# Kernel tuning notes

Measured on AMD Instinct MI355X. Metric: run time of the kernel, lower is better.

The kernel has to match this reference:

```python
import jax, jax.numpy as jnp
import numpy as np

DIM, HEADS, K = 128, 4, 7
HD = DIM // HEADS


def _nbr_idx(n, k):
    # NATTEN boundary-clamped neighborhood (dilation=1): window start clamped to [0, n-k]
    i = np.arange(n)
    start = np.clip(i - k // 2, 0, n - k)
    idx = start[:, None] + np.arange(k)[None, :]          # (n, k) absolute neighbor index
    rel = idx - i[:, None] + (k - 1)                      # (n, k) index into 2k-1 rpb axis
    return jnp.asarray(idx), jnp.asarray(rel)


def _ln(x, w, b, eps=1e-5):
    mu = jnp.mean(x, -1, keepdims=True)
    var = jnp.var(x, -1, keepdims=True)
    return (x - mu) * jax.lax.rsqrt(var + eps) * w + b


def setup_inputs() -> dict:
    key = jax.random.key(0)
    ks = jax.random.split(key, 16)
    B, H, W, C = 1, 128, 128, DIM
    f = jax.random.normal
    inp = {
        'x': f(ks[0], (B, H, W, C), jnp.float32),
        'y': f(ks[1], (B, H, W, C), jnp.float32),
        'qv_w': f(ks[2], (2 * C, C), jnp.float32) * 0.02,
        'qv_b': jnp.zeros((2 * C,), jnp.float32),
        'k_w': f(ks[3], (C, C), jnp.float32) * 0.02,
        'k_b': jnp.zeros((C,), jnp.float32),
        'rpb': f(ks[4], (HEADS, 2 * K - 1, 2 * K - 1), jnp.float32) * 0.02,
        'proj_w': f(ks[5], (C, C), jnp.float32) * 0.02,
        'proj_b': jnp.zeros((C,), jnp.float32),
        'n1_w': jnp.ones((C,), jnp.float32),
        'n1_b': jnp.zeros((C,), jnp.float32),
        'n2_w': jnp.ones((C,), jnp.float32),
        'n2_b': jnp.zeros((C,), jnp.float32),
        'fc1_w': f(ks[6], (4 * C, C), jnp.float32) * 0.02,
        'fc1_b': jnp.zeros((4 * C,), jnp.float32),
        'fc2_w': f(ks[7], (C, 4 * C), jnp.float32) * 0.02,
        'fc2_b': jnp.zeros((C,), jnp.float32),
    }
    return inp


def _block(x, y, qv_w, qv_b, k_w, k_b, rpb, proj_w, proj_b,
           n1_w, n1_b, n2_w, n2_b, fc1_w, fc1_b, fc2_w, fc2_b):
    B, H, W, C = x.shape
    scale = HD ** -0.5
    # ---- CrossNat2D attention on norm1(x) vs y ----
    xn = _ln(x, n1_w, n1_b)
    qv = xn @ qv_w.T + qv_b                               # (B,H,W,2C)
    q = qv[..., :C].reshape(B, H, W, HEADS, HD) * scale
    v = qv[..., C:].reshape(B, H, W, HEADS, HD)
    k = (y @ k_w.T + k_b).reshape(B, H, W, HEADS, HD)

    idx_h, rel_h = _nbr_idx(H, K)
    idx_w, rel_w = _nbr_idx(W, K)
    # gather neighborhoods: (B, H, K, W, K, HEADS, HD)
    k_nbr = k[:, idx_h][:, :, :, idx_w]
    v_nbr = v[:, idx_h][:, :, :, idx_w]

    # attention logits over KxK neighborhood
    attn = jnp.einsum('bijhd,biajchd->bijhac', q, k_nbr)  # (B,H,W,heads,K,K)
    bias = rpb[:, rel_h][..., rel_w]                      # (heads,H,K,W,K)
    attn = attn + jnp.transpose(bias, (1, 3, 0, 2, 4))    # broadcast over B
    attn = jax.nn.softmax(attn.reshape(B, H, W, HEADS, K * K), axis=-1)
    attn = attn.reshape(B, H, W, HEADS, K, K)

    out = jnp.einsum('bijhac,biajchd->bijhd', attn, v_nbr).reshape(B, H, W, C)
    out = out @ proj_w.T + proj_b

    x = x + out
    # ---- MLP ----
    h = _ln(x, n2_w, n2_b) @ fc1_w.T + fc1_b
    h = jax.nn.gelu(h, approximate=False) @ fc2_w.T + fc2_b
    return x + h


def reference(x, y, qv_w, qv_b, k_w, k_b, rpb, proj_w, proj_b,
              n1_w, n1_b, n2_w, n2_b, fc1_w, fc1_b, fc2_w, fc2_b):
    return _block(x, y, qv_w, qv_b, k_w, k_b, rpb, proj_w, proj_b,
                  n1_w, n1_b, n2_w, n2_b, fc1_w, fc1_b, fc2_w, fc2_b)
```

## Files before the change

kernel.cpp:

```cpp
#include <hip/hip_runtime.h>
#include <hip/hip_bf16.h>


#define N_PIX 16384
#define C 128
#define HEADS 4
#define HD 32
#define HW 128

typedef __hip_bfloat16 bf16;
typedef __attribute__((ext_vector_type(8))) short bf16x8;
typedef __attribute__((ext_vector_type(4))) float f32x4;

__device__ __forceinline__ short f2bs(float f) {
    bf16 h = __float2bfloat16(f);
    return (short)__bfloat16_as_ushort(h);
}
__device__ __forceinline__ float bs2f(short s) {
    __hip_bfloat16_raw r; r.x = (unsigned short)s;
    return __bfloat162float(__hip_bfloat16(r));
}
__device__ __forceinline__ float gelu_f(float v) {
    const float z = 1.5957691216f * (v + 0.044715f * v * v * v);
    return v / (1.f + __expf(-z));
}
__device__ __forceinline__ unsigned int pack2(float a, float b) {
    return (unsigned int)(unsigned short)f2bs(a) |
           ((unsigned int)(unsigned short)f2bs(b) << 16);
}

__global__ __launch_bounds__(256) void k_wconv(
    const float* __restrict__ qv_w, const float* __restrict__ k_w,
    const float* __restrict__ proj_w, const float* __restrict__ fc1_w,
    const float* __restrict__ fc2_w,
    short* __restrict__ wqv, short* __restrict__ wk, short* __restrict__ wproj,
    short* __restrict__ wfc1, short* __restrict__ wfc2) {
    const int i = blockIdx.x * 256 + threadIdx.x;
    if (i < 32768) wqv[i] = f2bs(qv_w[i]);
    if (i < 16384) { wk[i] = f2bs(k_w[i]); wproj[i] = f2bs(proj_w[i]); }
    if (i < 65536) { wfc1[i] = f2bs(fc1_w[i]); wfc2[i] = f2bs(fc2_w[i]); }
}

__global__ __launch_bounds__(256, 4) void k_qkv(
    const float* __restrict__ x, const float* __restrict__ y,
    const short* __restrict__ wqv, const float* __restrict__ qv_b,
    const short* __restrict__ wk, const float* __restrict__ k_b,
    const float* __restrict__ n1_w, const float* __restrict__ n1_b,
    bf16* __restrict__ qb, bf16* __restrict__ vb, bf16* __restrict__ kb) {
    __shared__ float xr[16][132];
    __shared__ short xn[16][136];
    __shared__ short yl[16][136];
    __shared__ float muA[16], riA[16];
    const int t = threadIdx.x;
    const int pix0 = (blockIdx.x & 7) * 2048 + (blockIdx.x >> 3) * 16;
    for (int e = t; e < 512; e += 256) {
        const int r = e >> 5, c4 = (e & 31) * 4;
        const float4 xv = *(const float4*)(x + (size_t)(pix0 + r) * C + c4);
        *(float4*)&xr[r][c4] = xv;
        const float4 yv = *(const float4*)(y + (size_t)(pix0 + r) * C + c4);
        uint2 yp; yp.x = pack2(yv.x, yv.y); yp.y = pack2(yv.z, yv.w);
        *(uint2*)&yl[r][c4] = yp;
    }
    __syncthreads();
    if (t < 128) {
        const int r = t >> 3, s = t & 7;
        float sm = 0.f, sq = 0.f;
        for (int i = 0; i < 16; i++) { float v = xr[r][s * 16 + i]; sm += v; sq += v * v; }
        for (int m = 1; m < 8; m <<= 1) { sm += __shfl_xor(sm, m, 64); sq += __shfl_xor(sq, m, 64); }
        if (s == 0) {
            const float mu = sm * (1.f / 128.f);
            const float var = sq * (1.f / 128.f) - mu * mu;
            muA[r] = mu; riA[r] = rsqrtf(var + 1e-5f);
        }
    }
    __syncthreads();
    for (int e = t; e < 2048; e += 256) {
        const int r = e >> 7, c = e & 127;
        xn[r][c] = f2bs((xr[r][c] - muA[r]) * riA[r] * n1_w[c] + n1_b[c]);
    }
    __syncthreads();
    const int wave = t >> 6, lane = t & 63, quad = lane >> 4, l15 = lane & 15;
    const float scale = 0.1767766952966369f;
    {
        bf16x8 aA[4];
#pragma unroll
        for (int kt = 0; kt < 4; kt++)
            aA[kt] = *(const bf16x8*)&xn[l15][kt * 32 + quad * 8];
#pragma unroll
        for (int s = 0; s < 4; s++) {
            const int n = (wave * 4 + s) * 16 + l15;
            f32x4 acc = {0.f, 0.f, 0.f, 0.f};
#pragma unroll
            for (int kt = 0; kt < 4; kt++) {
                bf16x8 b = *(const bf16x8*)&wqv[n * C + kt * 32 + quad * 8];
                acc = __builtin_amdgcn_mfma_f32_16x16x32_bf16(aA[kt], b, acc, 0, 0, 0);
            }
            const float bias = qv_b[n];
#pragma unroll
            for (int r = 0; r < 4; r++) {
                const int m = quad * 4 + r;
                const float v = acc[r] + bias;
                if (n < C) qb[(size_t)(pix0 + m) * C + n] = __float2bfloat16(v * scale);
                else       vb[(size_t)(pix0 + m) * C + (n - C)] = __float2bfloat16(v);
            }
        }
    }
    {
        bf16x8 aY[4];
#pragma unroll
        for (int kt = 0; kt < 4; kt++)
            aY[kt] = *(const bf16x8*)&yl[l15][kt * 32 + quad * 8];
        const int n0 = (wave * 2) * 16 + l15, n1 = (wave * 2 + 1) * 16 + l15;
        f32x4 a0 = {0.f, 0.f, 0.f, 0.f}, a1 = {0.f, 0.f, 0.f, 0.f};
#pragma unroll
        for (int kt = 0; kt < 4; kt++) {
            bf16x8 b0 = *(const bf16x8*)&wk[n0 * C + kt * 32 + quad * 8];
            bf16x8 b1 = *(const bf16x8*)&wk[n1 * C + kt * 32 + quad * 8];
            a0 = __builtin_amdgcn_mfma_f32_16x16x32_bf16(aY[kt], b0, a0, 0, 0, 0);
            a1 = __builtin_amdgcn_mfma_f32_16x16x32_bf16(aY[kt], b1, a1, 0, 0, 0);
        }
        const float b0s = k_b[n0], b1s = k_b[n1];
#pragma unroll
        for (int r = 0; r < 4; r++) {
            const int m = quad * 4 + r;
            kb[(size_t)(pix0 + m) * C + n0] = __float2bfloat16(a0[r] + b0s);
            kb[(size_t)(pix0 + m) * C + n1] = __float2bfloat16(a1[r] + b1s);
        }
    }
}

__global__ __launch_bounds__(256, 3) void k_attn(
    const bf16* __restrict__ qb, const bf16* __restrict__ kb,
    const bf16* __restrict__ vb, const float* __restrict__ rpb,
    const float* __restrict__ x,
    const short* __restrict__ wproj, const float* __restrict__ proj_b,
    float* __restrict__ out) {
    __shared__ short U[112 * 132];
    __shared__ short Pb[64 * 120];
    __shared__ short aoL[16 * 136];
    const int t = threadIdx.x;
    const int wave = t >> 6, lane = t & 63, quad = lane >> 4, l15 = lane & 15;
    const int h = wave;
    const int tile = (blockIdx.x & 7) * 128 + (blockIdx.x >> 3);
    const int i0 = (tile >> 5) * 4, j0 = (tile & 31) * 4;
    const int rs = min(max(i0 - 3, 0), 118);
    const int cs = min(max(j0 - 3, 0), 118);
    const int pA = (i0 + (l15 >> 2)) * HW + j0 + (l15 & 3);
    const bf16x8 aQ = *(const bf16x8*)(qb + (size_t)pA * C + h * HD + quad * 8);
    const int nR0 = h * 16 + l15, nR1 = (h + 4) * 16 + l15;
    float xres0[4], xres1[4];
#pragma unroll
    for (int r = 0; r < 4; r++) {
        const int m = quad * 4 + r;
        const int p = (i0 + (m >> 2)) * HW + j0 + (m & 3);
        xres0[r] = x[(size_t)p * C + nR0];
        xres1[r] = x[(size_t)p * C + nR1];
    }
    uint4 vst[7];
#pragma unroll
    for (int it = 0; it < 7; ++it) {
        const int u = t + it * 256;
        const int r = u >> 4, seg = u & 15;
        const int sr = min(r, 99);
        const size_t g = (size_t)((rs + sr / 10) * HW + cs + sr % 10) * C + seg * 8;
        *(uint4*)&U[r * 132 + seg * 8] = *(const uint4*)(kb + g);
        vst[it] = *(const uint4*)(vb + g);
    }
    __syncthreads();
    f32x4 S[7];
#pragma unroll
    for (int nt = 0; nt < 7; nt++) {
        const bf16x8 bK = *(const bf16x8*)&U[(nt * 16 + l15) * 132 + h * HD + quad * 8];
        f32x4 z = {0.f, 0.f, 0.f, 0.f};
        S[nt] = __builtin_amdgcn_mfma_f32_16x16x32_bf16(aQ, bK, z, 0, 0, 0);
    }
    __syncthreads();
#pragma unroll
    for (int it = 0; it < 7; ++it) {
        const int u = t + it * 256;
        const int r = u >> 4, seg = u & 15;
        *(uint4*)&U[r * 132 + seg * 8] = vst[it];
    }
    const float* rpbh = rpb + h * 169;
    int aiA[7], ajA[7];
#pragma unroll
    for (int nt = 0; nt < 7; nt++) {
        const int nb = nt * 16 + l15;
        aiA[nt] = rs + nb / 10;
        ajA[nt] = cs + nb % 10;
    }
    float smx[4];
#pragma unroll
    for (int r = 0; r < 4; r++) {
        const int m = quad * 4 + r;
        const int i = i0 + (m >> 2), j = j0 + (m & 3);
        const int shi = min(max(i - 3, 0), 121);
        const int swj = min(max(j - 3, 0), 121);
        float best = -1e30f;
#pragma unroll
        for (int nt = 0; nt < 7; nt++) {
            const int nb = nt * 16 + l15;
            const int ai = aiA[nt], aj = ajA[nt];
            const bool valid = (nb < 100) & (ai >= shi) & (ai <= shi + 6) & (aj >= swj) & (aj <= swj + 6);
            const int ri = min(max(ai - i + 6, 0), 12);
            const int rj = min(max(aj - j + 6, 0), 12);
            const float v = valid ? (S[nt][r] + rpbh[ri * 13 + rj]) : -1e30f;
            S[nt][r] = v;
            best = fmaxf(best, v);
        }
        for (int msk = 1; msk < 16; msk <<= 1) best = fmaxf(best, __shfl_xor(best, msk, 64));
        float s = 0.f;
#pragma unroll
        for (int nt = 0; nt < 7; nt++) {
            const float e = __expf(S[nt][r] - best);
            S[nt][r] = e;
            s += e;
        }
        for (int msk = 1; msk < 16; msk <<= 1) s += __shfl_xor(s, msk, 64);
        smx[r] = 1.f / s;
    }
#pragma unroll
    for (int r = 0; r < 4; r++) {
        short* prow = &Pb[(h * 16 + quad * 4 + r) * 120];
#pragma unroll
        for (int nt = 0; nt < 7; nt++) prow[nt * 16 + l15] = f2bs(S[nt][r] * smx[r]);
    }
    __syncthreads();
    f32x4 O0 = {0.f, 0.f, 0.f, 0.f}, O1 = {0.f, 0.f, 0.f, 0.f};
#pragma unroll
    for (int kt = 0; kt < 3; kt++) {
        const bf16x8 aP = *(const bf16x8*)&Pb[(h * 16 + l15) * 120 + kt * 32 + quad * 8];
#pragma unroll
        for (int nt2 = 0; nt2 < 2; nt2++) {
            const int ch = h * HD + nt2 * 16 + l15;
            const int base = (kt * 32 + quad * 8) * 132 + ch;
            bf16x8 bV;
#pragma unroll
            for (int jj = 0; jj < 8; jj++) bV[jj] = U[base + jj * 132];
            if (nt2 == 0) O0 = __builtin_amdgcn_mfma_f32_16x16x32_bf16(aP, bV, O0, 0, 0, 0);
            else          O1 = __builtin_amdgcn_mfma_f32_16x16x32_bf16(aP, bV, O1, 0, 0, 0);
        }
    }
    {
        bf16x8 aP = {0, 0, 0, 0, 0, 0, 0, 0};
        if (quad < 2) aP = *(const bf16x8*)&Pb[(h * 16 + l15) * 120 + 96 + quad * 8];
#pragma unroll
        for (int nt2 = 0; nt2 < 2; nt2++) {
            const int ch = h * HD + nt2 * 16 + l15;
            bf16x8 bV = {0, 0, 0, 0, 0, 0, 0, 0};
            if (quad < 2) {
                const int base = (96 + quad * 8) * 132 + ch;
#pragma unroll
                for (int jj = 0; jj < 8; jj++) bV[jj] = U[base + jj * 132];
            }
            if (nt2 == 0) O0 = __builtin_amdgcn_mfma_f32_16x16x32_bf16(aP, bV, O0, 0, 0, 0);
            else          O1 = __builtin_amdgcn_mfma_f32_16x16x32_bf16(aP, bV, O1, 0, 0, 0);
        }
    }
#pragma unroll
    for (int r = 0; r < 4; r++) {
        const int m = quad * 4 + r;
        aoL[m * 136 + h * HD + l15] = f2bs(O0[r]);
        aoL[m * 136 + h * HD + 16 + l15] = f2bs(O1[r]);
    }
    __syncthreads();
    bf16x8 aO[4];
#pragma unroll
    for (int kt = 0; kt < 4; kt++)
        aO[kt] = *(const bf16x8*)&aoL[l15 * 136 + kt * 32 + quad * 8];
    f32x4 a0 = {0.f, 0.f, 0.f, 0.f}, a1 = {0.f, 0.f, 0.f, 0.f};
#pragma unroll
    for (int kt = 0; kt < 4; kt++) {
        bf16x8 b0 = *(const bf16x8*)&wproj[nR0 * C + kt * 32 + quad * 8];
        bf16x8 b1 = *(const bf16x8*)&wproj[nR1 * C + kt * 32 + quad * 8];
        a0 = __builtin_amdgcn_mfma_f32_16x16x32_bf16(aO[kt], b0, a0, 0, 0, 0);
        a1 = __builtin_amdgcn_mfma_f32_16x16x32_bf16(aO[kt], b1, a1, 0, 0, 0);
    }
    const float b0s = proj_b[nR0], b1s = proj_b[nR1];
#pragma unroll
    for (int r = 0; r < 4; r++) {
        const int m = quad * 4 + r;
        const int p = (i0 + (m >> 2)) * HW + j0 + (m & 3);
        out[(size_t)p * C + nR0] = xres0[r] + a0[r] + b0s;
        out[(size_t)p * C + nR1] = xres1[r] + a1[r] + b1s;
    }
}

__global__ __launch_bounds__(256, 4) void k_mlp(
    const float* __restrict__ n2_w, const float* __restrict__ n2_b,
    const short* __restrict__ wfc1, const float* __restrict__ fc1_b,
    const short* __restrict__ wfc2, const float* __restrict__ fc2_b,
    float* __restrict__ out) {
    __shared__ float x1l[16][132];
    __shared__ short xnb[16][136];
    __shared__ short hb[16 * 520];
    __shared__ float muA[16], riA[16];
    const int t = threadIdx.x;
    const int pix0 = (blockIdx.x & 7) * 2048 + (blockIdx.x >> 3) * 16;
    for (int e = t; e < 512; e += 256) {
        const int r = e >> 5, c4 = (e & 31) * 4;
        *(float4*)&x1l[r][c4] = *(const float4*)(out + (size_t)(pix0 + r) * C + c4);
    }
    __syncthreads();
    if (t < 128) {
        const int r = t >> 3, s = t & 7;
        float sm = 0.f, sq = 0.f;
        for (int i = 0; i < 16; i++) { float v = x1l[r][s * 16 + i]; sm += v; sq += v * v; }
        for (int m = 1; m < 8; m <<= 1) { sm += __shfl_xor(sm, m, 64); sq += __shfl_xor(sq, m, 64); }
        if (s == 0) {
            const float mu = sm * (1.f / 128.f);
            const float var = sq * (1.f / 128.f) - mu * mu;
            muA[r] = mu; riA[r] = rsqrtf(var + 1e-5f);
        }
    }
    __syncthreads();
    for (int e = t; e < 2048; e += 256) {
        const int r = e >> 7, c = e & 127;
        xnb[r][c] = f2bs((x1l[r][c] - muA[r]) * riA[r] * n2_w[c] + n2_b[c]);
    }
    __syncthreads();
    const int wave = t >> 6, lane = t & 63, quad = lane >> 4, l15 = lane & 15;
    {
        bf16x8 aX[4];
#pragma unroll
        for (int kt = 0; kt < 4; kt++)
            aX[kt] = *(const bf16x8*)&xnb[l15][kt * 32 + quad * 8];
#pragma unroll
        for (int a = 0; a < 8; a++) {
            const int n = (wave * 8 + a) * 16 + l15;
            f32x4 acc = {0.f, 0.f, 0.f, 0.f};
#pragma unroll
            for (int kt = 0; kt < 4; kt++) {
                bf16x8 bw = *(const bf16x8*)&wfc1[n * C + kt * 32 + quad * 8];
                acc = __builtin_amdgcn_mfma_f32_16x16x32_bf16(aX[kt], bw, acc, 0, 0, 0);
            }
            const float bias = fc1_b[n];
#pragma unroll
            for (int r = 0; r < 4; r++) {
                const int m = quad * 4 + r;
                hb[m * 520 + n] = f2bs(gelu_f(acc[r] + bias));
            }
        }
    }
    __syncthreads();
    {
        const int n0 = (wave * 2) * 16 + l15, n1 = (wave * 2 + 1) * 16 + l15;
        f32x4 a0 = {0.f, 0.f, 0.f, 0.f}, a1 = {0.f, 0.f, 0.f, 0.f};
#pragma unroll
        for (int kt = 0; kt < 16; kt++) {
            const bf16x8 aP = *(const bf16x8*)&hb[l15 * 520 + kt * 32 + quad * 8];
            bf16x8 b0 = *(const bf16x8*)&wfc2[n0 * 512 + kt * 32 + quad * 8];
            bf16x8 b1 = *(const bf16x8*)&wfc2[n1 * 512 + kt * 32 + quad * 8];
            a0 = __builtin_amdgcn_mfma_f32_16x16x32_bf16(aP, b0, a0, 0, 0, 0);
            a1 = __builtin_amdgcn_mfma_f32_16x16x32_bf16(aP, b1, a1, 0, 0, 0);
        }
        const float b0s = fc2_b[n0], b1s = fc2_b[n1];
#pragma unroll
        for (int r = 0; r < 4; r++) {
            const int m = quad * 4 + r;
            out[(size_t)(pix0 + m) * C + n0] = a0[r] + b0s + x1l[m][n0];
            out[(size_t)(pix0 + m) * C + n1] = a1[r] + b1s + x1l[m][n1];
        }
    }
}

extern "C" void kernel_launch(void* const* d_in, const int* in_sizes, int n_in,
                              void* d_out, int out_size, void* d_ws, size_t ws_size,
                              hipStream_t stream) {
    const float* x      = (const float*)d_in[0];
    const float* y      = (const float*)d_in[1];
    const float* qv_w   = (const float*)d_in[2];
    const float* qv_b   = (const float*)d_in[3];
    const float* k_w    = (const float*)d_in[4];
    const float* k_b    = (const float*)d_in[5];
    const float* rpb    = (const float*)d_in[6];
    const float* proj_w = (const float*)d_in[7];
    const float* proj_b = (const float*)d_in[8];
    const float* n1_w   = (const float*)d_in[9];
    const float* n1_b   = (const float*)d_in[10];
    const float* n2_w   = (const float*)d_in[11];
    const float* n2_b   = (const float*)d_in[12];
    const float* fc1_w  = (const float*)d_in[13];
    const float* fc1_b  = (const float*)d_in[14];
    const float* fc2_w  = (const float*)d_in[15];
    const float* fc2_b  = (const float*)d_in[16];
    float* out = (float*)d_out;

    bf16* qb  = (bf16*)d_ws;
    bf16* vb  = qb + (size_t)N_PIX * C;
    bf16* kb  = vb + (size_t)N_PIX * C;
    short* wqv  = (short*)(kb + (size_t)N_PIX * C);
    short* wk   = wqv + 32768;
    short* wproj= wk + 16384;
    short* wfc1 = wproj + 16384;
    short* wfc2 = wfc1 + 65536;

    k_wconv<<<256, 256, 0, stream>>>(qv_w, k_w, proj_w, fc1_w, fc2_w,
                                     wqv, wk, wproj, wfc1, wfc2);
    k_qkv<<<1024, 256, 0, stream>>>(x, y, wqv, qv_b, wk, k_b, n1_w, n1_b,
                                    qb, vb, kb);
    k_attn<<<1024, 256, 0, stream>>>(qb, kb, vb, rpb, x, wproj, proj_b, out);
    k_mlp<<<1024, 256, 0, stream>>>(n2_w, n2_b, wfc1, fc1_b, wfc2, fc2_b, out);
}
```

Baseline: 177.4 us.

## Fuse attention, projection and MLP into one kernel with shuffle-based softmax

Merges the attention and MLP kernels into a single kernel, so the post-attention residual stays on chip and is never written to and re-read from global memory. The first QK MFMA now uses swapped operands so each lane holds one query's scores, which makes the softmax reductions cross-quad only. P is passed into the PV MFMA by register shuffles instead of a shared-memory round trip. Shared memory is aliased into a single buffer to allow four blocks per SM. The trade-off is that the LayerNorm-2 statistics are now computed from bf16-rounded residual values, and the kernel is longer with more barriers.

```diff
diff --git a/kernel.cpp b/kernel.cpp
--- a/kernel.cpp
+++ b/kernel.cpp
@@ -11,6 +11,8 @@
 typedef __hip_bfloat16 bf16;
 typedef __attribute__((ext_vector_type(8))) short bf16x8;
 typedef __attribute__((ext_vector_type(4))) float f32x4;
+
+union U32x4 { unsigned int u[4]; bf16x8 b; };
 
 __device__ __forceinline__ short f2bs(float f) {
     bf16 h = __float2bfloat16(f);
@@ -129,15 +131,21 @@
     }
 }
 
-__global__ __launch_bounds__(256, 3) void k_attn(
+__global__ __launch_bounds__(256, 4) void k_fam(
     const bf16* __restrict__ qb, const bf16* __restrict__ kb,
     const bf16* __restrict__ vb, const float* __restrict__ rpb,
     const float* __restrict__ x,
     const short* __restrict__ wproj, const float* __restrict__ proj_b,
+    const float* __restrict__ n2_w, const float* __restrict__ n2_b,
+    const short* __restrict__ wfc1, const float* __restrict__ fc1_b,
+    const short* __restrict__ wfc2, const float* __restrict__ fc2_b,
     float* __restrict__ out) {
-    __shared__ short U[112 * 132];
-    __shared__ short Pb[64 * 120];
-    __shared__ short aoL[16 * 136];
+    __shared__ short U[14784];
+    __shared__ float muA[16], riA[16];
+    short* const aoL = U;
+    short* const x1b = U + 2176;
+    short* const xnb = U + 4288;
+    short* const hb  = U + 6464;
     const int t = threadIdx.x;
     const int wave = t >> 6, lane = t & 63, quad = lane >> 4, l15 = lane & 15;
     const int h = wave;
@@ -172,7 +180,7 @@
     for (int nt = 0; nt < 7; nt++) {
         const bf16x8 bK = *(const bf16x8*)&U[(nt * 16 + l15) * 132 + h * HD + quad * 8];
         f32x4 z = {0.f, 0.f, 0.f, 0.f};
-        S[nt] = __builtin_amdgcn_mfma_f32_16x16x32_bf16(aQ, bK, z, 0, 0, 0);
+        S[nt] = __builtin_amdgcn_mfma_f32_16x16x32_bf16(bK, aQ, z, 0, 0, 0);
     }
     __syncthreads();
 #pragma unroll
@@ -182,54 +190,59 @@
         *(uint4*)&U[r * 132 + seg * 8] = vst[it];
     }
     const float* rpbh = rpb + h * 169;
-    int aiA[7], ajA[7];
+    const int ii = i0 + (l15 >> 2), jj0_ = j0 + (l15 & 3);
+    const int shi = min(max(ii - 3, 0), 121);
+    const int swj = min(max(jj0_ - 3, 0), 121);
+    float best = -1e30f;
 #pragma unroll
     for (int nt = 0; nt < 7; nt++) {
-        const int nb = nt * 16 + l15;
-        aiA[nt] = rs + nb / 10;
-        ajA[nt] = cs + nb % 10;
-    }
-    float smx[4];
-#pragma unroll
-    for (int r = 0; r < 4; r++) {
-        const int m = quad * 4 + r;
-        const int i = i0 + (m >> 2), j = j0 + (m & 3);
-        const int shi = min(max(i - 3, 0), 121);
-        const int swj = min(max(j - 3, 0), 121);
-        float best = -1e30f;
-#pragma unroll
-        for (int nt = 0; nt < 7; nt++) {
-            const int nb = nt * 16 + l15;
-            const int ai = aiA[nt], aj = ajA[nt];
+#pragma unroll
+        for (int r = 0; r < 4; r++) {
+            const int nb = nt * 16 + quad * 4 + r;
+            const int ai = rs + nb / 10, aj = cs + nb % 10;
             const bool valid = (nb < 100) & (ai >= shi) & (ai <= shi + 6) & (aj >= swj) & (aj <= swj + 6);
-            const int ri = min(max(ai - i + 6, 0), 12);
-            const int rj = min(max(aj - j + 6, 0), 12);
+            const int ri = min(max(ai - ii + 6, 0), 12);
+            const int rj = min(max(aj - jj0_ + 6, 0), 12);
             const float v = valid ? (S[nt][r] + rpbh[ri * 13 + rj]) : -1e30f;
             S[nt][r] = v;
             best = fmaxf(best, v);
         }
-        for (int msk = 1; msk < 16; msk <<= 1) best = fmaxf(best, __shfl_xor(best, msk, 64));
-        float s = 0.f;
-#pragma unroll
-        for (int nt = 0; nt < 7; nt++) {
+    }
+    best = fmaxf(best, __shfl_xor(best, 16, 64));
+    best = fmaxf(best, __shfl_xor(best, 32, 64));
+    float s = 0.f;
+#pragma unroll
+    for (int nt = 0; nt < 7; nt++) {
+#pragma unroll
+        for (int r = 0; r < 4; r++) {
             const float e = __expf(S[nt][r] - best);
             S[nt][r] = e;
             s += e;
         }
-        for (int msk = 1; msk < 16; msk <<= 1) s += __shfl_xor(s, msk, 64);
-        smx[r] = 1.f / s;
-    }
-#pragma unroll
-    for (int r = 0; r < 4; r++) {
-        short* prow = &Pb[(h * 16 + quad * 4 + r) * 120];
-#pragma unroll
-        for (int nt = 0; nt < 7; nt++) prow[nt * 16 + l15] = f2bs(S[nt][r] * smx[r]);
+    }
+    s += __shfl_xor(s, 16, 64);
+    s += __shfl_xor(s, 32, 64);
+    const float smx = 1.f / s;
+    unsigned int pk[14];
+#pragma unroll
+    for (int nt = 0; nt < 7; nt++) {
+        pk[nt * 2]     = pack2(S[nt][0] * smx, S[nt][1] * smx);
+        pk[nt * 2 + 1] = pack2(S[nt][2] * smx, S[nt][3] * smx);
     }
     __syncthreads();
     f32x4 O0 = {0.f, 0.f, 0.f, 0.f}, O1 = {0.f, 0.f, 0.f, 0.f};
 #pragma unroll
     for (int kt = 0; kt < 3; kt++) {
-        const bf16x8 aP = *(const bf16x8*)&Pb[(h * 16 + l15) * 120 + kt * 32 + quad * 8];
+        U32x4 uu;
+#pragma unroll
+        for (int w = 0; w < 4; w++) {
+            const int qs = ((quad & 1) << 1) + (w >> 1);
+            const int src = (qs << 4) | l15;
+            const unsigned va = __shfl(pk[4 * kt + (w & 1)], src, 64);
+            const unsigned vb2 = __shfl(pk[4 * kt + 2 + (w & 1)], src, 64);
+            uu.u[w] = (quad >> 1) ? vb2 : va;
+        }
+        const bf16x8 aP = uu.b;
 #pragma unroll
         for (int nt2 = 0; nt2 < 2; nt2++) {
             const int ch = h * HD + nt2 * 16 + l15;
@@ -242,8 +255,15 @@
         }
     }
     {
-        bf16x8 aP = {0, 0, 0, 0, 0, 0, 0, 0};
-        if (quad < 2) aP = *(const bf16x8*)&Pb[(h * 16 + l15) * 120 + 96 + quad * 8];
+        U32x4 uu;
+#pragma unroll
+        for (int w = 0; w < 4; w++) {
+            const int qs = ((quad & 1) << 1) + (w >> 1);
+            const int src = (qs << 4) | l15;
+            const unsigned va = __shfl(pk[12 + (w & 1)], src, 64);
+            uu.u[w] = (quad >> 1) ? 0u : va;
+        }
+        const bf16x8 aP = uu.b;
 #pragma unroll
         for (int nt2 = 0; nt2 < 2; nt2++) {
             const int ch = h * HD + nt2 * 16 + l15;
@@ -257,6 +277,7 @@
             else          O1 = __builtin_amdgcn_mfma_f32_16x16x32_bf16(aP, bV, O1, 0, 0, 0);
         }
     }
+    __syncthreads();
 #pragma unroll
     for (int r = 0; r < 4; r++) {
         const int m = quad * 4 + r;
@@ -264,50 +285,38 @@
         aoL[m * 136 + h * HD + 16 + l15] = f2bs(O1[r]);
     }
     __syncthreads();
-    bf16x8 aO[4];
-#pragma unroll
-    for (int kt = 0; kt < 4; kt++)
-        aO[kt] = *(const bf16x8*)&aoL[l15 * 136 + kt * 32 + quad * 8];
-    f32x4 a0 = {0.f, 0.f, 0.f, 0.f}, a1 = {0.f, 0.f, 0.f, 0.f};
-#pragma unroll
-    for (int kt = 0; kt < 4; kt++) {
-        bf16x8 b0 = *(const bf16x8*)&wproj[nR0 * C + kt * 32 + quad * 8];
-        bf16x8 b1 = *(const bf16x8*)&wproj[nR1 * C + kt * 32 + quad * 8];
-        a0 = __builtin_amdgcn_mfma_f32_16x16x32_bf16(aO[kt], b0, a0, 0, 0, 0);
-        a1 = __builtin_amdgcn_mfma_f32_16x16x32_bf16(aO[kt], b1, a1, 0, 0, 0);
-    }
-    const float b0s = proj_b[nR0], b1s = proj_b[nR1];
-#pragma unroll
-    for (int r = 0; r < 4; r++) {
-        const int m = quad * 4 + r;
-        const int p = (i0 + (m >> 2)) * HW + j0 + (m & 3);
-        out[(size_t)p * C + nR0] = xres0[r] + a0[r] + b0s;
-        out[(size_t)p * C + nR1] = xres1[r] + a1[r] + b1s;
-    }
-}
-
-__global__ __launch_bounds__(256, 4) void k_mlp(
-    const float* __restrict__ n2_w, const float* __restrict__ n2_b,
-    const short* __restrict__ wfc1, const float* __restrict__ fc1_b,
-    const short* __restrict__ wfc2, const float* __restrict__ fc2_b,
-    float* __restrict__ out) {
-    __shared__ float x1l[16][132];
-    __shared__ short xnb[16][136];
-    __shared__ short hb[16 * 520];
-    __shared__ float muA[16], riA[16];
-    const int t = threadIdx.x;
-    const int pix0 = (blockIdx.x & 7) * 2048 + (blockIdx.x >> 3) * 16;
-    for (int e = t; e < 512; e += 256) {
-        const int r = e >> 5, c4 = (e & 31) * 4;
-        *(float4*)&x1l[r][c4] = *(const float4*)(out + (size_t)(pix0 + r) * C + c4);
+    float x1f0[4], x1f1[4];
+    {
+        bf16x8 aO[4];
+#pragma unroll
+        for (int kt = 0; kt < 4; kt++)
+            aO[kt] = *(const bf16x8*)&aoL[l15 * 136 + kt * 32 + quad * 8];
+        f32x4 a0 = {0.f, 0.f, 0.f, 0.f}, a1 = {0.f, 0.f, 0.f, 0.f};
+#pragma unroll
+        for (int kt = 0; kt < 4; kt++) {
+            bf16x8 b0 = *(const bf16x8*)&wproj[nR0 * C + kt * 32 + quad * 8];
+            bf16x8 b1 = *(const bf16x8*)&wproj[nR1 * C + kt * 32 + quad * 8];
+            a0 = __builtin_amdgcn_mfma_f32_16x16x32_bf16(aO[kt], b0, a0, 0, 0, 0);
+            a1 = __builtin_amdgcn_mfma_f32_16x16x32_bf16(aO[kt], b1, a1, 0, 0, 0);
+        }
+        const float b0s = proj_b[nR0], b1s = proj_b[nR1];
+#pragma unroll
+        for (int r = 0; r < 4; r++) {
+            const int m = quad * 4 + r;
+            const float v0 = xres0[r] + a0[r] + b0s;
+            const float v1 = xres1[r] + a1[r] + b1s;
+            x1f0[r] = v0; x1f1[r] = v1;
+            x1b[m * 132 + nR0] = f2bs(v0);
+            x1b[m * 132 + nR1] = f2bs(v1);
+        }
     }
     __syncthreads();
     if (t < 128) {
-        const int r = t >> 3, s = t & 7;
+        const int r = t >> 3, s2 = t & 7;
         float sm = 0.f, sq = 0.f;
-        for (int i = 0; i < 16; i++) { float v = x1l[r][s * 16 + i]; sm += v; sq += v * v; }
+        for (int i2 = 0; i2 < 16; i2++) { float v = bs2f(x1b[r * 132 + s2 * 16 + i2]); sm += v; sq += v * v; }
         for (int m = 1; m < 8; m <<= 1) { sm += __shfl_xor(sm, m, 64); sq += __shfl_xor(sq, m, 64); }
-        if (s == 0) {
+        if (s2 == 0) {
             const float mu = sm * (1.f / 128.f);
             const float var = sq * (1.f / 128.f) - mu * mu;
             muA[r] = mu; riA[r] = rsqrtf(var + 1e-5f);
@@ -316,15 +325,14 @@
     __syncthreads();
     for (int e = t; e < 2048; e += 256) {
         const int r = e >> 7, c = e & 127;
-        xnb[r][c] = f2bs((x1l[r][c] - muA[r]) * riA[r] * n2_w[c] + n2_b[c]);
-    }
-    __syncthreads();
-    const int wave = t >> 6, lane = t & 63, quad = lane >> 4, l15 = lane & 15;
+        xnb[r * 136 + c] = f2bs((bs2f(x1b[r * 132 + c]) - muA[r]) * riA[r] * n2_w[c] + n2_b[c]);
+    }
+    __syncthreads();
     {
         bf16x8 aX[4];
 #pragma unroll
         for (int kt = 0; kt < 4; kt++)
-            aX[kt] = *(const bf16x8*)&xnb[l15][kt * 32 + quad * 8];
+            aX[kt] = *(const bf16x8*)&xnb[l15 * 136 + kt * 32 + quad * 8];
 #pragma unroll
         for (int a = 0; a < 8; a++) {
             const int n = (wave * 8 + a) * 16 + l15;
@@ -344,22 +352,22 @@
     }
     __syncthreads();
     {
-        const int n0 = (wave * 2) * 16 + l15, n1 = (wave * 2 + 1) * 16 + l15;
         f32x4 a0 = {0.f, 0.f, 0.f, 0.f}, a1 = {0.f, 0.f, 0.f, 0.f};
 #pragma unroll
         for (int kt = 0; kt < 16; kt++) {
             const bf16x8 aP = *(const bf16x8*)&hb[l15 * 520 + kt * 32 + quad * 8];
-            bf16x8 b0 = *(const bf16x8*)&wfc2[n0 * 512 + kt * 32 + quad * 8];
-            bf16x8 b1 = *(const bf16x8*)&wfc2[n1 * 512 + kt * 32 + quad * 8];
+            bf16x8 b0 = *(const bf16x8*)&wfc2[nR0 * 512 + kt * 32 + quad * 8];
+            bf16x8 b1 = *(const bf16x8*)&wfc2[nR1 * 512 + kt * 32 + quad * 8];
             a0 = __builtin_amdgcn_mfma_f32_16x16x32_bf16(aP, b0, a0, 0, 0, 0);
             a1 = __builtin_amdgcn_mfma_f32_16x16x32_bf16(aP, b1, a1, 0, 0, 0);
         }
-        const float b0s = fc2_b[n0], b1s = fc2_b[n1];
+        const float b0s = fc2_b[nR0], b1s = fc2_b[nR1];
 #pragma unroll
         for (int r = 0; r < 4; r++) {
             const int m = quad * 4 + r;
-            out[(size_t)(pix0 + m) * C + n0] = a0[r] + b0s + x1l[m][n0];
-            out[(size_t)(pix0 + m) * C + n1] = a1[r] + b1s + x1l[m][n1];
+            const int p = (i0 + (m >> 2)) * HW + j0 + (m & 3);
+            out[(size_t)p * C + nR0] = a0[r] + b0s + x1f0[r];
+            out[(size_t)p * C + nR1] = a1[r] + b1s + x1f1[r];
         }
     }
 }
@@ -399,6 +407,6 @@
                                      wqv, wk, wproj, wfc1, wfc2);
     k_qkv<<<1024, 256, 0, stream>>>(x, y, wqv, qv_b, wk, k_b, n1_w, n1_b,
                                     qb, vb, kb);
-    k_attn<<<1024, 256, 0, stream>>>(qb, kb, vb, rpb, x, wproj, proj_b, out);
-    k_mlp<<<1024, 256, 0, stream>>>(n2_w, n2_b, wfc1, fc1_b, wfc2, fc2_b, out);
-}
+    k_fam<<<1024, 256, 0, stream>>>(qb, kb, vb, rpb, x, wproj, proj_b, n2_w, n2_b,
+                                    wfc1, fc1_b, wfc2, fc2_b, out);
+}
```

After: 170.3 us. 4.0% less time.
